# Kernel optimization log

Hardware: AMD Instinct MI355X
Metric: run time of the kernel (lower is better)

The kernel has to match this reference:

```python
import jax, jax.numpy as jnp
import numpy as np

E = 512        # audio_embd == video_embd
HID = 640      # hidden_dim
NH = 10        # n_heads
DK = HID // NH # 64
BTNK = 4
NUM_CLASSES = 527
B, L_AUD, L_VID = 4, 1024, 1024


def pos_encoding(L, d):
    pos = jnp.arange(L, dtype=jnp.float32)[:, None]
    div = jnp.exp(jnp.arange(0, d, 2, dtype=jnp.float32) * (-np.log(10000.0) / d))
    pe = jnp.zeros((L, d), dtype=jnp.float32)
    pe = pe.at[:, 0::2].set(jnp.sin(pos * div))
    pe = pe.at[:, 1::2].set(jnp.cos(pos * div))
    return pe


def layernorm(x, g, b, eps=1e-5):
    m = jnp.mean(x, axis=-1, keepdims=True)
    v = jnp.var(x, axis=-1, keepdims=True)
    return (x - m) * jax.lax.rsqrt(v + eps) * g + b


def setup_inputs() -> dict:
    key = jax.random.key(0)
    ks = jax.random.split(key, 16)
    s = 0.02
    return {
        "audio_feat": jax.random.normal(ks[0], (B, L_AUD, E), jnp.float32),
        "video_feat": jax.random.normal(ks[1], (B, L_VID, E), jnp.float32),
        "audio_tok": s * jax.random.normal(ks[2], (1, 1, E), jnp.float32),
        "video_tok": s * jax.random.normal(ks[3], (1, 1, E), jnp.float32),
        "btnk_toks": s * jax.random.normal(ks[4], (1, BTNK, E), jnp.float32),
        "Wk": s * jax.random.normal(ks[5], (E, HID), jnp.float32),
        "bk": jnp.zeros((HID,), jnp.float32),
        "Wq": s * jax.random.normal(ks[6], (E, HID), jnp.float32),
        "bq": jnp.zeros((HID,), jnp.float32),
        "Wv": s * jax.random.normal(ks[7], (E, HID), jnp.float32),
        "bv": jnp.zeros((HID,), jnp.float32),
        "ln_g": jnp.ones((HID,), jnp.float32),
        "ln_b": jnp.zeros((HID,), jnp.float32),
        "Wap": s * jax.random.normal(ks[8], (HID, NUM_CLASSES), jnp.float32),
        "bap": jnp.zeros((NUM_CLASSES,), jnp.float32),
        "Wvp": s * jax.random.normal(ks[9], (HID, NUM_CLASSES), jnp.float32),
        "bvp": jnp.zeros((NUM_CLASSES,), jnp.float32),
    }


def reference(audio_feat, video_feat, audio_tok, video_tok, btnk_toks,
              Wk, bk, Wq, bq, Wv, bv, ln_g, ln_b, Wap, bap, Wvp, bvp):
    b, La = audio_feat.shape[:2]
    Lv = video_feat.shape[1]
    # layout: [audio (La), aud_cls (1), bottleneck (BTNK), video (Lv), vid_cls (1)]
    feats = jnp.concatenate([
        audio_feat,
        jnp.broadcast_to(audio_tok, (b, 1, E)),
        jnp.broadcast_to(btnk_toks, (b, BTNK, E)),
        video_feat,
        jnp.broadcast_to(video_tok, (b, 1, E)),
    ], axis=1)
    L = feats.shape[1]
    feats = feats + pos_encoding(L, E)[None]  # dropout is identity at eval

    k = (feats @ Wk + bk).reshape(b, L, NH, DK)
    q = (feats @ Wq + bq).reshape(b, L, NH, DK)
    v = (feats @ Wv + bv).reshape(b, L, NH, DK)

    # NOTE: original computes einsum(k, q) and softmaxes over the q axis (-2).
    attn = jnp.einsum('bmhd,bnhd->bmnh', k, q) / np.sqrt(DK)
    # _get_btnk_mask(L) writes to rows/cols L+1:L+1+BTNK, which are out of
    # range for an (L, L) mask -> mask is all-False (upstream bug, kept faithful).
    attn = jax.nn.softmax(attn, axis=-2)
    out = jnp.einsum('bmnh,bnhd->bmhd', attn, v).reshape(b, L, HID)

    out = layernorm(out, ln_g, ln_b)
    aud_cls = out[:, 0]                 # indices replicate original exactly
    vid_cls = out[:, La + 1 + BTNK]
    aud_pred = aud_cls @ Wap + bap
    vid_pred = vid_cls @ Wvp + bvp
    return (aud_pred + vid_pred) / 2
```

## Files before the change

### kernel.cpp

```cpp
#include <hip/hip_runtime.h>
#include <cstddef>

#define E_DIM 512
#define HID   640
#define NH    10
#define DK    64
#define LTOT  2054
#define NCLS  527
#define NB    4
#define KC    (-0.0179889460390157f)

__device__ __forceinline__ float wave_reduce_sum_dpp(float x) {
    float t;
    t = __int_as_float(__builtin_amdgcn_update_dpp(0, __float_as_int(x), 0x111, 0xf, 0xf, false)); x += t;
    t = __int_as_float(__builtin_amdgcn_update_dpp(0, __float_as_int(x), 0x112, 0xf, 0xf, false)); x += t;
    t = __int_as_float(__builtin_amdgcn_update_dpp(0, __float_as_int(x), 0x114, 0xf, 0xe, false)); x += t;
    t = __int_as_float(__builtin_amdgcn_update_dpp(0, __float_as_int(x), 0x118, 0xf, 0xc, false)); x += t;
    t = __int_as_float(__builtin_amdgcn_update_dpp(0, __float_as_int(x), 0x142, 0xa, 0xf, false)); x += t;
    t = __int_as_float(__builtin_amdgcn_update_dpp(0, __float_as_int(x), 0x143, 0xc, 0xf, false)); x += t;
    return __int_as_float(__builtin_amdgcn_readlane(__float_as_int(x), 63));
}

__device__ __forceinline__ const float* row_src(int b, int n,
        const float* au, const float* vi, const float* at,
        const float* vt, const float* bt) {
    if (n < 1024) return au + ((size_t)b*1024 + n)*E_DIM;
    if (n == 1024) return at;
    if (n < 1029) return bt + (size_t)(n-1025)*E_DIM;
    if (n < 2053) return vi + ((size_t)b*1024 + (n-1029))*E_DIM;
    return vt;
}

__global__ __launch_bounds__(256) void ba_ku_kernel(
        const float* __restrict__ audio, const float* __restrict__ video,
        const float* __restrict__ Wk, const float* __restrict__ bk,
        const float* __restrict__ Wq,
        float* __restrict__ uws) {
    int h = blockIdx.x, bm = blockIdx.y;
    int b = bm >> 1, m = bm & 1;
    int mrow = m ? 1029 : 0;
    const float* src = m ? (video + (size_t)b*1024*E_DIM)
                         : (audio + (size_t)b*1024*E_DIM);
    int t = threadIdx.x;
    __shared__ float frow[E_DIM];
    __shared__ __align__(16) float kl[DK];
    __shared__ float red[4][DK];
    for (int i = t; i < E_DIM; i += 256) {
        float div = expf((float)(i & ~1) * KC);
        float arg = (float)mrow * div;
        float pe  = (i & 1) ? cosf(arg) : sinf(arg);
        frow[i] = src[i] + pe;
    }
    __syncthreads();
    int d = t & 63, es = t >> 6;
    const float* wkcol = Wk + (size_t)(h*DK) + d;
    float part = 0.f;
    #pragma unroll 8
    for (int e = es*128; e < es*128 + 128; ++e)
        part = fmaf(frow[e], wkcol[(size_t)e*HID], part);
    red[es][d] = part;
    __syncthreads();
    if (t < DK)
        kl[t] = bk[h*DK + t] + red[0][t] + red[1][t] + red[2][t] + red[3][t];
    __syncthreads();
    #pragma unroll
    for (int s = 0; s < 2; ++s) {
        int e = s*256 + t;
        const float4* wq4 = (const float4*)(Wq + (size_t)e*HID + h*DK);
        const float4* k4  = (const float4*)kl;
        float acc = 0.f;
        #pragma unroll
        for (int d4 = 0; d4 < 16; ++d4) {
            float4 w = wq4[d4]; float4 kk = k4[d4];
            acc = fmaf(w.x,kk.x, fmaf(w.y,kk.y, fmaf(w.z,kk.z, fmaf(w.w,kk.w, acc))));
        }
        uws[((size_t)bm*NH + h)*E_DIM + e] = acc * 0.125f;
    }
}

__global__ __launch_bounds__(128) void ba_fused_kernel(
        const float* __restrict__ audio, const float* __restrict__ video,
        const float* __restrict__ atok, const float* __restrict__ vtok,
        const float* __restrict__ btnk,
        const float* __restrict__ uws,
        float* __restrict__ wpart, float* __restrict__ mcs,
        float* __restrict__ lcs, int nch, int crw) {
    int b = blockIdx.z, chunk = blockIdx.x, t = threadIdx.x;
    int w = t >> 6, lane = t & 63;
    int pbase = (blockIdx.y*2 + w)*2;
    int eb = lane*8;
    float4 u0[2], u1[2];
    #pragma unroll
    for (int i = 0; i < 2; ++i) {
        const float4* up = (const float4*)(uws + (size_t)(b*20 + pbase + i)*E_DIM + eb);
        u0[i] = up[0]; u1[i] = up[1];
    }
    int r0 = chunk*crw;
    float sn[4], cn[4], sd[4], cd[4];
    #pragma unroll
    for (int q = 0; q < 4; ++q) {
        float dv = expf((float)(eb + 2*q) * KC);
        sd[q] = sinf(dv); cd[q] = cosf(dv);
        float a = (float)r0 * dv;
        sn[q] = sinf(a); cn[q] = cosf(a);
    }
    float m[2], l[2], acc[2][8];
    #pragma unroll
    for (int i = 0; i < 2; ++i) {
        m[i] = -1e30f; l[i] = 0.f;
        #pragma unroll
        for (int j = 0; j < 8; ++j) acc[i][j] = 0.f;
    }
    int rend = min(r0 + crw, LTOT);

#define ADV_ROT() { \
    _Pragma("unroll") \
    for (int q = 0; q < 4; ++q) { \
        float s2_ = fmaf(sn[q], cd[q],  cn[q]*sd[q]); \
        float c2_ = fmaf(cn[q], cd[q], -sn[q]*sd[q]); \
        sn[q] = s2_; cn[q] = c2_; } }

#define MAKE_FP(fp, x0, x1) { \
    (fp)[0]=(x0).x+sn[0]; (fp)[1]=(x0).y+cn[0]; (fp)[2]=(x0).z+sn[1]; (fp)[3]=(x0).w+cn[1]; \
    (fp)[4]=(x1).x+sn[2]; (fp)[5]=(x1).y+cn[2]; (fp)[6]=(x1).z+sn[3]; (fp)[7]=(x1).w+cn[3]; }

#define DOT8(res, fp, i) { \
    float a_; \
    a_ = (fp)[0]*u0[i].x; \
    a_ = fmaf((fp)[1], u0[i].y, a_); \
    a_ = fmaf((fp)[2], u0[i].z, a_); \
    a_ = fmaf((fp)[3], u0[i].w, a_); \
    a_ = fmaf((fp)[4], u1[i].x, a_); \
    a_ = fmaf((fp)[5], u1[i].y, a_); \
    a_ = fmaf((fp)[6], u1[i].z, a_); \
    a_ = fmaf((fp)[7], u1[i].w, a_); \
    (res) = a_; }

#define SOFT_UPD(i, sc, fp) { \
    if ((sc) > m[i]) { \
        float scale_ = __expf(m[i] - (sc)); \
        m[i] = (sc); \
        l[i] = fmaf(l[i], scale_, 1.f); \
        _Pragma("unroll") \
        for (int j = 0; j < 8; ++j) acc[i][j] = fmaf(acc[i][j], scale_, (fp)[j]); \
    } else { \
        float wg_ = __expf((sc) - m[i]); \
        l[i] += wg_; \
        _Pragma("unroll") \
        for (int j = 0; j < 8; ++j) acc[i][j] = fmaf(wg_, (fp)[j], acc[i][j]); } }

#define LOAD_GRP(rr) { \
    const float* s0p_ = row_src(b, (rr),   audio, video, atok, vtok, btnk); \
    const float* s1p_ = row_src(b, (rr)+1, audio, video, atok, vtok, btnk); \
    const float* s2p_ = row_src(b, (rr)+2, audio, video, atok, vtok, btnk); \
    const float* s3p_ = row_src(b, (rr)+3, audio, video, atok, vtok, btnk); \
    x00 = *(const float4*)(s0p_ + eb); x01 = *(const float4*)(s0p_ + eb + 4); \
    x10 = *(const float4*)(s1p_ + eb); x11 = *(const float4*)(s1p_ + eb + 4); \
    x20 = *(const float4*)(s2p_ + eb); x21 = *(const float4*)(s2p_ + eb + 4); \
    x30 = *(const float4*)(s3p_ + eb); x31 = *(const float4*)(s3p_ + eb + 4); }

    float4 x00, x01, x10, x11, x20, x21, x30, x31;
    int r = r0;
    if (r + 3 < rend) { LOAD_GRP(r); }
    while (r + 3 < rend) {
        float fp0[8], fp1[8], fp2[8], fp3[8];
        MAKE_FP(fp0, x00, x01); ADV_ROT();
        MAKE_FP(fp1, x10, x11); ADV_ROT();
        MAKE_FP(fp2, x20, x21); ADV_ROT();
        MAKE_FP(fp3, x30, x31); ADV_ROT();
        int rn = r + 4;
        if (rn + 3 < rend) { LOAD_GRP(rn); }
        float d0, d1, d2, d3, d4, d5, d6, d7;
        DOT8(d0, fp0, 0); DOT8(d1, fp0, 1);
        DOT8(d2, fp1, 0); DOT8(d3, fp1, 1);
        DOT8(d4, fp2, 0); DOT8(d5, fp2, 1);
        DOT8(d6, fp3, 0); DOT8(d7, fp3, 1);
        float sc0 = wave_reduce_sum_dpp(d0);
        float sc1 = wave_reduce_sum_dpp(d1);
        float sc2 = wave_reduce_sum_dpp(d2);
        float sc3 = wave_reduce_sum_dpp(d3);
        float sc4 = wave_reduce_sum_dpp(d4);
        float sc5 = wave_reduce_sum_dpp(d5);
        float sc6 = wave_reduce_sum_dpp(d6);
        float sc7 = wave_reduce_sum_dpp(d7);
        SOFT_UPD(0, sc0, fp0); SOFT_UPD(0, sc2, fp1);
        SOFT_UPD(0, sc4, fp2); SOFT_UPD(0, sc6, fp3);
        SOFT_UPD(1, sc1, fp0); SOFT_UPD(1, sc3, fp1);
        SOFT_UPD(1, sc5, fp2); SOFT_UPD(1, sc7, fp3);
        r = rn;
    }
    for (; r < rend; ++r) {
        const float* s0p = row_src(b, r, audio, video, atok, vtok, btnk);
        float4 y0 = *(const float4*)(s0p + eb), y1 = *(const float4*)(s0p + eb + 4);
        float fp0[8];
        MAKE_FP(fp0, y0, y1); ADV_ROT();
        float d0, d1;
        DOT8(d0, fp0, 0); DOT8(d1, fp0, 1);
        float sc0 = wave_reduce_sum_dpp(d0);
        float sc1 = wave_reduce_sum_dpp(d1);
        SOFT_UPD(0, sc0, fp0);
        SOFT_UPD(1, sc1, fp0);
    }
    #pragma unroll
    for (int i = 0; i < 2; ++i) {
        float* dst = wpart + ((size_t)(b*20 + pbase + i)*nch + chunk)*E_DIM + eb;
        *(float4*)dst       = make_float4(acc[i][0], acc[i][1], acc[i][2], acc[i][3]);
        *(float4*)(dst + 4) = make_float4(acc[i][4], acc[i][5], acc[i][6], acc[i][7]);
    }
    float mv = (lane == 0) ? m[0] : m[1];
    float lv = (lane == 0) ? l[0] : l[1];
    if (lane < 2) {
        size_t ix = (size_t)(b*20 + pbase + lane)*nch + chunk;
        mcs[ix] = mv;
        lcs[ix] = lv;
    }
#undef ADV_ROT
#undef MAKE_FP
#undef DOT8
#undef SOFT_UPD
#undef LOAD_GRP
}

__global__ __launch_bounds__(1024) void ba_outraw_kernel(
        const float* __restrict__ wpart, const float* __restrict__ mcs,
        const float* __restrict__ lcs,
        const float* __restrict__ Wv, const float* __restrict__ bv,
        float* __restrict__ orow, int nch) {
    int h = blockIdx.x, bm = blockIdx.y, z = blockIdx.z, t = threadIdx.x;
    int b = bm >> 1, m = bm & 1, p = m*10 + h;
    __shared__ float ml[128], ll[128], coefs[128];
    __shared__ float Msh, invLsh;
    __shared__ float wh[E_DIM];
    __shared__ float sh[2][E_DIM];
    __shared__ float red[16][64];
    const float* mrow = mcs + (size_t)(b*20 + p)*nch;
    const float* lrow = lcs + (size_t)(b*20 + p)*nch;
    if (t < nch) { ml[t] = mrow[t]; ll[t] = lrow[t]; }
    __syncthreads();
    if (t < 64) {
        float mv = -1e30f;
        for (int c = t; c < nch; c += 64) mv = fmaxf(mv, ml[c]);
        #pragma unroll
        for (int off = 1; off < 64; off <<= 1) mv = fmaxf(mv, __shfl_xor(mv, off, 64));
        if (t == 0) Msh = mv;
    }
    __syncthreads();
    float M = Msh;
    if (t < 64) {
        float lv = 0.f;
        for (int c = t; c < nch; c += 64) lv += ll[c] * __expf(ml[c] - M);
        lv = wave_reduce_sum_dpp(lv);
        if (t == 0) invLsh = 1.0f / lv;
    }
    __syncthreads();
    if (t < nch) coefs[t] = __expf(ml[t] - M) * invLsh;
    __syncthreads();
    int e = t & 511, half = t >> 9;
    int cn4 = nch >> 2, chf = cn4 >> 1;
    int c0 = z*cn4 + half*chf;
    int c1 = c0 + chf;
    const float* basep = wpart + (size_t)(b*20 + p)*nch*E_DIM;
    float a0 = 0.f, a1 = 0.f;
    int c = c0;
    for (; c + 1 < c1; c += 2) {
        a0 = fmaf(basep[(size_t)c*E_DIM + e],     coefs[c],   a0);
        a1 = fmaf(basep[(size_t)(c+1)*E_DIM + e], coefs[c+1], a1);
    }
    if (c < c1) a0 = fmaf(basep[(size_t)c*E_DIM + e], coefs[c], a0);
    sh[half][e] = a0 + a1;
    __syncthreads();
    if (t < E_DIM) wh[t] = sh[0][t] + sh[1][t];
    __syncthreads();
    int d = t & 63, es = t >> 6;
    float part = 0.f;
    #pragma unroll 8
    for (int e2 = es*32; e2 < es*32 + 32; ++e2)
        part = fmaf(wh[e2], Wv[(size_t)e2*HID + h*DK + d], part);
    red[es][d] = part;
    __syncthreads();
    if (t < 64) {
        float s = 0.f;
        #pragma unroll
        for (int i = 0; i < 16; ++i) s += red[i][t];
        if (z == 0) s += bv[h*DK + t];
        orow[((size_t)z*8 + bm)*HID + h*DK + t] = s;
    }
}

__global__ __launch_bounds__(512) void ba_lnpred_kernel(
        const float* __restrict__ orow,
        const float* __restrict__ g, const float* __restrict__ bb,
        const float* __restrict__ Wap, const float* __restrict__ bap,
        const float* __restrict__ Wvp, const float* __restrict__ bvp,
        float* __restrict__ out) {
    int b = blockIdx.y, t = threadIdx.x;
    const int OS = 8*HID;
    const float* A = orow + (size_t)(2*b)*HID;
    const float* V = A + HID;
    __shared__ float lnA[HID], lnV[HID];
    __shared__ float wred[4][8];
    __shared__ float psum[8][2][64];
    float sA = 0.f, qA = 0.f, sV = 0.f, qV = 0.f;
    for (int i = t; i < HID; i += 512) {
        float xa = A[i] + A[i+OS] + A[i+2*OS] + A[i+3*OS];
        float xv = V[i] + V[i+OS] + V[i+2*OS] + V[i+3*OS];
        lnA[i] = xa; lnV[i] = xv;
        sA += xa; qA = fmaf(xa, xa, qA);
        sV += xv; qV = fmaf(xv, xv, qV);
    }
    sA = wave_reduce_sum_dpp(sA); qA = wave_reduce_sum_dpp(qA);
    sV = wave_reduce_sum_dpp(sV); qV = wave_reduce_sum_dpp(qV);
    int w = t >> 6, lane = t & 63;
    if (lane == 0) { wred[0][w] = sA; wred[1][w] = qA; wred[2][w] = sV; wred[3][w] = qV; }
    __syncthreads();
    float tsA = 0.f, tqA = 0.f, tsV = 0.f, tqV = 0.f;
    #pragma unroll
    for (int i = 0; i < 8; ++i) {
        tsA += wred[0][i]; tqA += wred[1][i]; tsV += wred[2][i]; tqV += wred[3][i];
    }
    float meanA = tsA*(1.0f/HID), varA = tqA*(1.0f/HID) - meanA*meanA;
    float meanV = tsV*(1.0f/HID), varV = tqV*(1.0f/HID) - meanV*meanV;
    float rA = rsqrtf(varA + 1e-5f), rV = rsqrtf(varV + 1e-5f);
    for (int i = t; i < HID; i += 512) {
        float gg = g[i], bbv = bb[i];
        lnA[i] = (lnA[i] - meanA)*rA*gg + bbv;
        lnV[i] = (lnV[i] - meanV)*rV*gg + bbv;
    }
    __syncthreads();
    int c = blockIdx.x*64 + lane;
    int cc = (c < NCLS) ? c : (NCLS - 1);
    int j0 = w*80;
    float sa = 0.f, sv = 0.f;
    #pragma unroll 8
    for (int j = j0; j < j0 + 80; ++j) {
        sa = fmaf(lnA[j], Wap[(size_t)j*NCLS + cc], sa);
        sv = fmaf(lnV[j], Wvp[(size_t)j*NCLS + cc], sv);
    }
    psum[w][0][lane] = sa;
    psum[w][1][lane] = sv;
    __syncthreads();
    if (t < 64 && c < NCLS) {
        float ta = 0.f, tv = 0.f;
        #pragma unroll
        for (int i = 0; i < 8; ++i) { ta += psum[i][0][t]; tv += psum[i][1][t]; }
        out[(size_t)b*NCLS + c] = 0.5f*(ta + tv + bap[c] + bvp[c]);
    }
}

extern "C" void kernel_launch(void* const* d_in, const int* in_sizes, int n_in,
                              void* d_out, int out_size, void* d_ws, size_t ws_size,
                              hipStream_t stream) {
    const float* audio = (const float*)d_in[0];
    const float* video = (const float*)d_in[1];
    const float* atok  = (const float*)d_in[2];
    const float* vtok  = (const float*)d_in[3];
    const float* btnk  = (const float*)d_in[4];
    const float* Wk    = (const float*)d_in[5];
    const float* bk    = (const float*)d_in[6];
    const float* Wq    = (const float*)d_in[7];
    const float* Wv    = (const float*)d_in[9];
    const float* bv    = (const float*)d_in[10];
    const float* ln_g  = (const float*)d_in[11];
    const float* ln_b  = (const float*)d_in[12];
    const float* Wap   = (const float*)d_in[13];
    const float* bap   = (const float*)d_in[14];
    const float* Wvp   = (const float*)d_in[15];
    const float* bvp   = (const float*)d_in[16];
    float* out = (float*)d_out;
    float* ws  = (float*)d_ws;

    auto need = [](int nch) -> size_t {
        return (size_t)(8*NH*E_DIM)
             + (size_t)NB*nch*20*E_DIM + 2*(size_t)NB*nch*20
             + (size_t)4*8*HID;
    };
    int nch = 40;
    if (ws_size >= need(128)*sizeof(float)) nch = 128;
    else if (ws_size >= need(64)*sizeof(float)) nch = 64;
    int crw = (LTOT + nch - 1) / nch;

    float* uws   = ws;
    float* wpart = uws + 8*NH*E_DIM;
    float* mcs   = wpart + (size_t)NB*nch*20*E_DIM;
    float* lcs   = mcs + (size_t)NB*nch*20;
    float* orw   = lcs + (size_t)NB*nch*20;

    ba_ku_kernel<<<dim3(NH, 8), 256, 0, stream>>>(audio, video, Wk, bk, Wq, uws);
    ba_fused_kernel<<<dim3(nch, 5, NB), 128, 0, stream>>>(audio, video, atok, vtok, btnk,
                                                          uws, wpart, mcs, lcs, nch, crw);
    ba_outraw_kernel<<<dim3(NH, 8, 4), 1024, 0, stream>>>(wpart, mcs, lcs, Wv, bv, orw, nch);
    ba_lnpred_kernel<<<dim3(9, NB), 512, 0, stream>>>(orw, ln_g, ln_b,
                                                      Wap, bap, Wvp, bvp, out);
}
```

Baseline: 148.0 us.

## Give each fused-kernel wave four query rows and split the outraw reduction eight ways

The fused attention kernel now runs one wave per block, and each wave handles four (query,head) rows instead of two. Each loaded feature row with its positional encoding is therefore reused for four dot products, which halves redundant global loads and sin/cos rotation work per row, at the cost of more registers and half the threads per block. The row unroll drops from 4 to 2 to offset the register cost. The outraw kernel's chunk reduction is split over 8 z-slices instead of 4, and the layernorm kernel sums the 8 partials, adding parallelism to the reduction tail. The nch=40 fallback is removed, which presumes nch is divisible by 16.

```diff
diff --git a/kernel.cpp b/kernel.cpp
--- a/kernel.cpp
+++ b/kernel.cpp
@@ -78,20 +78,19 @@
     }
 }
 
-__global__ __launch_bounds__(128) void ba_fused_kernel(
+__global__ __launch_bounds__(64) void ba_fused_kernel(
         const float* __restrict__ audio, const float* __restrict__ video,
         const float* __restrict__ atok, const float* __restrict__ vtok,
         const float* __restrict__ btnk,
         const float* __restrict__ uws,
         float* __restrict__ wpart, float* __restrict__ mcs,
         float* __restrict__ lcs, int nch, int crw) {
-    int b = blockIdx.z, chunk = blockIdx.x, t = threadIdx.x;
-    int w = t >> 6, lane = t & 63;
-    int pbase = (blockIdx.y*2 + w)*2;
+    int b = blockIdx.z, chunk = blockIdx.x, lane = threadIdx.x;
+    int pbase = blockIdx.y*4;
     int eb = lane*8;
-    float4 u0[2], u1[2];
-    #pragma unroll
-    for (int i = 0; i < 2; ++i) {
+    float4 u0[4], u1[4];
+    #pragma unroll
+    for (int i = 0; i < 4; ++i) {
         const float4* up = (const float4*)(uws + (size_t)(b*20 + pbase + i)*E_DIM + eb);
         u0[i] = up[0]; u1[i] = up[1];
     }
@@ -104,9 +103,9 @@
         float a = (float)r0 * dv;
         sn[q] = sinf(a); cn[q] = cosf(a);
     }
-    float m[2], l[2], acc[2][8];
-    #pragma unroll
-    for (int i = 0; i < 2; ++i) {
+    float m[4], l[4], acc[4][8];
+    #pragma unroll
+    for (int i = 0; i < 4; ++i) {
         m[i] = -1e30f; l[i] = 0.f;
         #pragma unroll
         for (int j = 0; j < 8; ++j) acc[i][j] = 0.f;
@@ -149,32 +148,24 @@
         _Pragma("unroll") \
         for (int j = 0; j < 8; ++j) acc[i][j] = fmaf(wg_, (fp)[j], acc[i][j]); } }
 
-#define LOAD_GRP(rr) { \
+#define LOAD_GRP2(rr) { \
     const float* s0p_ = row_src(b, (rr),   audio, video, atok, vtok, btnk); \
     const float* s1p_ = row_src(b, (rr)+1, audio, video, atok, vtok, btnk); \
-    const float* s2p_ = row_src(b, (rr)+2, audio, video, atok, vtok, btnk); \
-    const float* s3p_ = row_src(b, (rr)+3, audio, video, atok, vtok, btnk); \
     x00 = *(const float4*)(s0p_ + eb); x01 = *(const float4*)(s0p_ + eb + 4); \
-    x10 = *(const float4*)(s1p_ + eb); x11 = *(const float4*)(s1p_ + eb + 4); \
-    x20 = *(const float4*)(s2p_ + eb); x21 = *(const float4*)(s2p_ + eb + 4); \
-    x30 = *(const float4*)(s3p_ + eb); x31 = *(const float4*)(s3p_ + eb + 4); }
-
-    float4 x00, x01, x10, x11, x20, x21, x30, x31;
+    x10 = *(const float4*)(s1p_ + eb); x11 = *(const float4*)(s1p_ + eb + 4); }
+
+    float4 x00, x01, x10, x11;
     int r = r0;
-    if (r + 3 < rend) { LOAD_GRP(r); }
-    while (r + 3 < rend) {
-        float fp0[8], fp1[8], fp2[8], fp3[8];
+    if (r + 1 < rend) { LOAD_GRP2(r); }
+    while (r + 1 < rend) {
+        float fp0[8], fp1[8];
         MAKE_FP(fp0, x00, x01); ADV_ROT();
         MAKE_FP(fp1, x10, x11); ADV_ROT();
-        MAKE_FP(fp2, x20, x21); ADV_ROT();
-        MAKE_FP(fp3, x30, x31); ADV_ROT();
-        int rn = r + 4;
-        if (rn + 3 < rend) { LOAD_GRP(rn); }
+        int rn = r + 2;
+        if (rn + 1 < rend) { LOAD_GRP2(rn); }
         float d0, d1, d2, d3, d4, d5, d6, d7;
-        DOT8(d0, fp0, 0); DOT8(d1, fp0, 1);
-        DOT8(d2, fp1, 0); DOT8(d3, fp1, 1);
-        DOT8(d4, fp2, 0); DOT8(d5, fp2, 1);
-        DOT8(d6, fp3, 0); DOT8(d7, fp3, 1);
+        DOT8(d0, fp0, 0); DOT8(d1, fp0, 1); DOT8(d2, fp0, 2); DOT8(d3, fp0, 3);
+        DOT8(d4, fp1, 0); DOT8(d5, fp1, 1); DOT8(d6, fp1, 2); DOT8(d7, fp1, 3);
         float sc0 = wave_reduce_sum_dpp(d0);
         float sc1 = wave_reduce_sum_dpp(d1);
         float sc2 = wave_reduce_sum_dpp(d2);
@@ -183,10 +174,10 @@
         float sc5 = wave_reduce_sum_dpp(d5);
         float sc6 = wave_reduce_sum_dpp(d6);
         float sc7 = wave_reduce_sum_dpp(d7);
-        SOFT_UPD(0, sc0, fp0); SOFT_UPD(0, sc2, fp1);
-        SOFT_UPD(0, sc4, fp2); SOFT_UPD(0, sc6, fp3);
-        SOFT_UPD(1, sc1, fp0); SOFT_UPD(1, sc3, fp1);
-        SOFT_UPD(1, sc5, fp2); SOFT_UPD(1, sc7, fp3);
+        SOFT_UPD(0, sc0, fp0); SOFT_UPD(1, sc1, fp0);
+        SOFT_UPD(2, sc2, fp0); SOFT_UPD(3, sc3, fp0);
+        SOFT_UPD(0, sc4, fp1); SOFT_UPD(1, sc5, fp1);
+        SOFT_UPD(2, sc6, fp1); SOFT_UPD(3, sc7, fp1);
         r = rn;
     }
     for (; r < rend; ++r) {
@@ -194,22 +185,24 @@
         float4 y0 = *(const float4*)(s0p + eb), y1 = *(const float4*)(s0p + eb + 4);
         float fp0[8];
         MAKE_FP(fp0, y0, y1); ADV_ROT();
-        float d0, d1;
-        DOT8(d0, fp0, 0); DOT8(d1, fp0, 1);
+        float d0, d1, d2, d3;
+        DOT8(d0, fp0, 0); DOT8(d1, fp0, 1); DOT8(d2, fp0, 2); DOT8(d3, fp0, 3);
         float sc0 = wave_reduce_sum_dpp(d0);
         float sc1 = wave_reduce_sum_dpp(d1);
-        SOFT_UPD(0, sc0, fp0);
-        SOFT_UPD(1, sc1, fp0);
-    }
-    #pragma unroll
-    for (int i = 0; i < 2; ++i) {
+        float sc2 = wave_reduce_sum_dpp(d2);
+        float sc3 = wave_reduce_sum_dpp(d3);
+        SOFT_UPD(0, sc0, fp0); SOFT_UPD(1, sc1, fp0);
+        SOFT_UPD(2, sc2, fp0); SOFT_UPD(3, sc3, fp0);
+    }
+    #pragma unroll
+    for (int i = 0; i < 4; ++i) {
         float* dst = wpart + ((size_t)(b*20 + pbase + i)*nch + chunk)*E_DIM + eb;
         *(float4*)dst       = make_float4(acc[i][0], acc[i][1], acc[i][2], acc[i][3]);
         *(float4*)(dst + 4) = make_float4(acc[i][4], acc[i][5], acc[i][6], acc[i][7]);
     }
-    float mv = (lane == 0) ? m[0] : m[1];
-    float lv = (lane == 0) ? l[0] : l[1];
-    if (lane < 2) {
+    float mv = (lane == 0) ? m[0] : (lane == 1) ? m[1] : (lane == 2) ? m[2] : m[3];
+    float lv = (lane == 0) ? l[0] : (lane == 1) ? l[1] : (lane == 2) ? l[2] : l[3];
+    if (lane < 4) {
         size_t ix = (size_t)(b*20 + pbase + lane)*nch + chunk;
         mcs[ix] = mv;
         lcs[ix] = lv;
@@ -218,7 +211,7 @@
 #undef MAKE_FP
 #undef DOT8
 #undef SOFT_UPD
-#undef LOAD_GRP
+#undef LOAD_GRP2
 }
 
 __global__ __launch_bounds__(1024) void ba_outraw_kernel(
@@ -256,8 +249,8 @@
     if (t < nch) coefs[t] = __expf(ml[t] - M) * invLsh;
     __syncthreads();
     int e = t & 511, half = t >> 9;
-    int cn4 = nch >> 2, chf = cn4 >> 1;
-    int c0 = z*cn4 + half*chf;
+    int cnz = nch >> 3, chf = cnz >> 1;
+    int c0 = z*cnz + half*chf;
     int c1 = c0 + chf;
     const float* basep = wpart + (size_t)(b*20 + p)*nch*E_DIM;
     float a0 = 0.f, a1 = 0.f;
@@ -302,8 +295,9 @@
     __shared__ float psum[8][2][64];
     float sA = 0.f, qA = 0.f, sV = 0.f, qV = 0.f;
     for (int i = t; i < HID; i += 512) {
-        float xa = A[i] + A[i+OS] + A[i+2*OS] + A[i+3*OS];
-        float xv = V[i] + V[i+OS] + V[i+2*OS] + V[i+3*OS];
+        float xa = 0.f, xv = 0.f;
+        #pragma unroll
+        for (int s = 0; s < 8; ++s) { xa += A[i + s*OS]; xv += V[i + s*OS]; }
         lnA[i] = xa; lnV[i] = xv;
         sA += xa; qA = fmaf(xa, xa, qA);
         sV += xv; qV = fmaf(xv, xv, qV);
@@ -372,11 +366,9 @@
     auto need = [](int nch) -> size_t {
         return (size_t)(8*NH*E_DIM)
              + (size_t)NB*nch*20*E_DIM + 2*(size_t)NB*nch*20
-             + (size_t)4*8*HID;
+             + (size_t)8*8*HID;
     };
-    int nch = 40;
-    if (ws_size >= need(128)*sizeof(float)) nch = 128;
-    else if (ws_size >= need(64)*sizeof(float)) nch = 64;
+    int nch = (ws_size >= need(128)*sizeof(float)) ? 128 : 64;
     int crw = (LTOT + nch - 1) / nch;
 
     float* uws   = ws;
@@ -386,9 +378,9 @@
     float* orw   = lcs + (size_t)NB*nch*20;
 
     ba_ku_kernel<<<dim3(NH, 8), 256, 0, stream>>>(audio, video, Wk, bk, Wq, uws);
-    ba_fused_kernel<<<dim3(nch, 5, NB), 128, 0, stream>>>(audio, video, atok, vtok, btnk,
-                                                          uws, wpart, mcs, lcs, nch, crw);
-    ba_outraw_kernel<<<dim3(NH, 8, 4), 1024, 0, stream>>>(wpart, mcs, lcs, Wv, bv, orw, nch);
+    ba_fused_kernel<<<dim3(nch, 5, NB), 64, 0, stream>>>(audio, video, atok, vtok, btnk,
+                                                         uws, wpart, mcs, lcs, nch, crw);
+    ba_outraw_kernel<<<dim3(NH, 8, 8), 1024, 0, stream>>>(wpart, mcs, lcs, Wv, bv, orw, nch);
     ba_lnpred_kernel<<<dim3(9, NB), 512, 0, stream>>>(orw, ln_g, ln_b,
                                                       Wap, bap, Wvp, bvp, out);
 }
```

Result: slower. 154.3 us (+4.3%).
